# Kernel optimization log

Hardware: AMD Instinct MI355X
Metric: run time of the kernel (lower is better)

Reference implementation:

```python
import jax, jax.numpy as jnp
import numpy as np

N_NODES = 100000
N_EDGES = 3200000
D_IN = 128
D_HID = 32
D_OUT = 20
EPS = 1e-12  # matches torch F.normalize clamp


def setup_inputs() -> dict:
    key = jax.random.key(0)
    ks = jax.random.split(key, 10)
    x = jax.random.normal(ks[0], (N_NODES, D_IN), dtype=jnp.float32)
    edge_index = jax.random.randint(ks[1], (2, N_EDGES), 0, N_NODES, dtype=jnp.int32)
    def lin(k, fin, fout):
        return jax.random.normal(k, (fin, fout), dtype=jnp.float32) / np.float32(np.sqrt(fin))
    # SAGEConv: lin_l (applied to aggregated neighbors, has bias), lin_r (root, no bias)
    W1l = lin(ks[2], D_IN, D_HID); b1 = jnp.zeros((D_HID,), jnp.float32)
    W1r = lin(ks[3], D_IN, D_HID)
    W2l = lin(ks[4], D_HID, D_HID); b2 = jnp.zeros((D_HID,), jnp.float32)
    W2r = lin(ks[5], D_HID, D_HID)
    Wc = lin(ks[6], D_HID, D_OUT)
    bc = jax.random.normal(ks[7], (D_OUT,), dtype=jnp.float32) * 0.01
    return {"x": x, "edge_index": edge_index, "W1l": W1l, "b1": b1, "W1r": W1r,
            "W2l": W2l, "b2": b2, "W2r": W2r, "Wc": Wc, "bc": bc}


def _sage_conv(h, src, dst, Wl, bl, Wr):
    # mean aggregation of source features at destination nodes
    msgs = h[src]                                              # [E, d] gather
    agg = jax.ops.segment_sum(msgs, dst, num_segments=N_NODES)  # [N, d] scatter-add
    cnt = jax.ops.segment_sum(jnp.ones((src.shape[0],), h.dtype), dst, num_segments=N_NODES)
    mean = agg / jnp.maximum(cnt, 1.0)[:, None]
    out = mean @ Wl + bl + h @ Wr                              # combine neighbor + root
    norm = jnp.linalg.norm(out, axis=-1, keepdims=True)
    return out / jnp.maximum(norm, EPS)                        # L2 normalize


def reference(x, edge_index, W1l, b1, W1r, W2l, b2, W2r, Wc, bc):
    src, dst = edge_index[0], edge_index[1]
    h = jnp.tanh(_sage_conv(x, src, dst, W1l, b1, W1r))
    h = jnp.tanh(_sage_conv(h, src, dst, W2l, b2, W2r))
    out = jax.nn.log_softmax(h @ Wc + bc, axis=1)
    return (out, h)
```

## Files before the change

kernel.cpp:

```cpp
#include <hip/hip_runtime.h>
#include <hip/hip_fp16.h>
#include <cmath>

constexpr int NN   = 100000;
constexpr int NE   = 3200000;
constexpr int DIN  = 128;
constexpr int DH   = 32;
constexpr int DOUT = 20;

constexpr int NB    = 392;
constexpr int NBUSE = (NN + 255) / 256;
constexpr int NBLK  = 256;
constexpr int SLICE = NE / NBLK;

constexpr int NPB = 64;
constexpr int XSB = 136;
constexpr int HSS = 36;

typedef __attribute__((ext_vector_type(8))) short short8v;
typedef __attribute__((ext_vector_type(4))) float f32x4;

__device__ inline unsigned short f2bf(float f) {
    unsigned u = __builtin_bit_cast(unsigned, f);
    unsigned r = 0x7FFFu + ((u >> 16) & 1u);
    return (unsigned short)((u + r) >> 16);
}

__device__ inline unsigned f2fp8(float f) {
    unsigned u = __builtin_bit_cast(unsigned, f);
    unsigned s = (u >> 24) & 0x80u;
    unsigned au = u & 0x7fffffffu;
    if (au > 0x43E00000u) au = 0x43E00000u;
    unsigned u2 = au + 0x7FFFFu + ((au >> 20) & 1u);
    int em = (int)(u2 >> 20) - (120 << 3);
    em = em < 0 ? 0 : (em > 0x7E ? 0x7E : em);
    return s | (unsigned)em;
}
__device__ inline float dec8(unsigned b) {
    unsigned r = ((b & 0x80u) << 24) | (((b & 0x7fu) << 20) + 0x3C000000u);
    return __builtin_bit_cast(float, r);
}

__global__ __launch_bounds__(256, 4) void lin1_kernel(
    const float* __restrict__ x, const float* __restrict__ Wl,
    const float* __restrict__ Wr, unsigned char* __restrict__ xlf8,
    float* __restrict__ xr)
{
    __shared__ unsigned short xs[NPB * XSB];
    int t = threadIdx.x;
    int nodeBase = blockIdx.x * NPB;

    const float4* x4 = reinterpret_cast<const float4*>(x) + (size_t)nodeBase * (DIN / 4);
    for (int i = t; i < NPB * (DIN / 4); i += 256) {
        int n = i >> 5, c = i & 31;
        float4 v = make_float4(0.f, 0.f, 0.f, 0.f);
        if (nodeBase + n < NN) v = x4[i];
        unsigned lo = (unsigned)f2bf(v.x) | ((unsigned)f2bf(v.y) << 16);
        unsigned hi = (unsigned)f2bf(v.z) | ((unsigned)f2bf(v.w) << 16);
        *reinterpret_cast<uint2*>(&xs[n * XSB + c * 4]) = make_uint2(lo, hi);
    }
    __syncthreads();

    int wv   = t >> 6;
    int lane = t & 63;
    const float* W = (wv & 2) ? Wr : Wl;
    int jbase = (wv & 1) * 16;
    int ncol  = jbase + (lane & 15);
    int krow  = (lane >> 4) * 8;

    short8v bfrag[4];
#pragma unroll
    for (int ks = 0; ks < 4; ++ks) {
        const float* wp = W + (ks * 32 + krow) * DH + ncol;
        short8v f;
#pragma unroll
        for (int e = 0; e < 8; ++e) f[e] = (short)f2bf(wp[e * DH]);
        bfrag[ks] = f;
    }

    f32x4 acc[4];
#pragma unroll
    for (int m = 0; m < 4; ++m) acc[m] = f32x4{0.f, 0.f, 0.f, 0.f};

#pragma unroll
    for (int m = 0; m < 4; ++m) {
        int row = m * 16 + (lane & 15);
#pragma unroll
        for (int ks = 0; ks < 4; ++ks) {
            short8v a = *reinterpret_cast<const short8v*>(&xs[row * XSB + ks * 32 + krow]);
            acc[m] = __builtin_amdgcn_mfma_f32_16x16x32_bf16(a, bfrag[ks], acc[m], 0, 0, 0);
        }
    }

#pragma unroll
    for (int m = 0; m < 4; ++m) {
        int rbase = m * 16 + (lane >> 4) * 4;
#pragma unroll
        for (int r = 0; r < 4; ++r) {
            int node = nodeBase + rbase + r;
            if (node < NN) {
                float v = acc[m][r];
                if (wv & 2) xr[(size_t)node * DH + ncol] = v;
                else        xlf8[(size_t)node * DH + ncol] = (unsigned char)f2fp8(v);
            }
        }
    }
}

__global__ __launch_bounds__(1024) void countA_kernel(
    const int* __restrict__ ei, int* __restrict__ counts)
{
    __shared__ int h[NB];
    int blk = blockIdx.x, t = threadIdx.x;
    for (int i = t; i < NB; i += 1024) h[i] = 0;
    __syncthreads();
    int base = blk * SLICE;
    for (int i = base + t; i < base + SLICE; i += 1024) {
        int dst = ei[NE + i];
        atomicAdd(&h[dst >> 8], 1);
    }
    __syncthreads();
    for (int i = t; i < NB; i += 1024) counts[blk * NB + i] = h[i];
}

__global__ __launch_bounds__(256) void scanB1_kernel(
    const int* __restrict__ counts, int* __restrict__ offs, int* __restrict__ totals)
{
    __shared__ int sdata[256];
    int b = blockIdx.x, t = threadIdx.x;
    int v = counts[t * NB + b];
    int tp = (t & 7) * 32 + (t >> 3);
    sdata[tp] = v;
    __syncthreads();
    for (int off = 1; off < 256; off <<= 1) {
        int tmp = (t >= off) ? sdata[t - off] : 0;
        __syncthreads();
        sdata[t] += tmp;
        __syncthreads();
    }
    offs[b * 256 + t] = sdata[tp] - v;
    if (t == 255) totals[b] = sdata[255];
}

__global__ void scanB2_kernel(const int* __restrict__ totals, int* __restrict__ bases,
                              int* __restrict__ start)
{
    if (threadIdx.x == 0 && blockIdx.x == 0) {
        int acc = 0;
        for (int i = 0; i < NB; ++i) { bases[i] = acc; acc += totals[i]; }
        bases[NB] = acc;
        start[NN] = acc;
    }
}

__global__ __launch_bounds__(1024) void scatterC_kernel(
    const int* __restrict__ ei, const int* __restrict__ offs,
    const int* __restrict__ bases, unsigned* __restrict__ csrtmp)
{
    __shared__ int cnt[NB];
    __shared__ int wbase[NB];
    int blk = blockIdx.x, t = threadIdx.x;
    for (int i = t; i < NB; i += 1024) {
        cnt[i] = 0;
        wbase[i] = bases[i] + offs[i * 256 + blk];
    }
    __syncthreads();
    int base = blk * SLICE;
    for (int i = base + t; i < base + SLICE; i += 1024) {
        int dst = ei[NE + i];
        int src = ei[i];
        int b = dst >> 8;
        int r = atomicAdd(&cnt[b], 1);
        csrtmp[wbase[b] + r] = ((unsigned)(dst & 255) << 17) | (unsigned)src;
    }
}

__global__ __launch_bounds__(1024) void regroupD_kernel(
    const unsigned* __restrict__ csrtmp, const int* __restrict__ bases,
    int* __restrict__ csrsrc, int* __restrict__ start)
{
    __shared__ int h[256];
    __shared__ int sdata[256];
    int b = blockIdx.x, t = threadIdx.x;
    int lo = bases[b], hi = bases[b + 1];
    if (t < 256) h[t] = 0;
    __syncthreads();
    for (int i = lo + t; i < hi; i += 1024)
        atomicAdd(&h[csrtmp[i] >> 17], 1);
    __syncthreads();
    int v = 0;
    if (t < 256) { v = h[t]; sdata[t] = v; }
    __syncthreads();
    for (int off = 1; off < 256; off <<= 1) {
        int tmp = 0;
        if (t < 256 && t >= off) tmp = sdata[t - off];
        __syncthreads();
        if (t < 256) sdata[t] += tmp;
        __syncthreads();
    }
    if (t < 256) {
        int ex = sdata[t] - v;
        int node = b * 256 + t;
        if (node < NN) start[node] = lo + ex;
        h[t] = ex;
    }
    __syncthreads();
    for (int i = lo + t; i < hi; i += 1024) {
        unsigned u = csrtmp[i];
        int r = atomicAdd(&h[u >> 17], 1);
        csrsrc[lo + r] = (int)(u & 0x1FFFFu);
    }
}

__device__ inline float4 gather_core(const int* __restrict__ csrsrc,
                                     const unsigned* __restrict__ feat8,
                                     int s, int e, unsigned c)
{
    __half2 zero2 = __float2half2_rn(0.f);
    __half2 p0a = zero2, p0b = zero2, p1a = zero2, p1b = zero2;
    __half2 p2a = zero2, p2b = zero2, p3a = zero2, p3b = zero2;
    int i = s;
    for (; i + 8 <= e; i += 8) {
        unsigned off[8];
#pragma unroll
        for (int q = 0; q < 8; ++q) off[q] = (unsigned)csrsrc[i + q] * 8u + c;
        unsigned vv[8];
#pragma unroll
        for (int q = 0; q < 8; ++q) vv[q] = feat8[off[q]];
#pragma unroll
        for (int q = 0; q < 8; ++q) {
            unsigned w = vv[q];
            unsigned p01 = __builtin_amdgcn_perm(0u, w, 0x04010400u);
            unsigned p23 = __builtin_amdgcn_perm(0u, w, 0x04030402u);
            unsigned h01 = ((p01 & 0x00800080u) << 8) |
                           (((p01 << 7) & 0x3F803F80u) + 0x20002000u);
            unsigned h23 = ((p23 & 0x00800080u) << 8) |
                           (((p23 << 7) & 0x3F803F80u) + 0x20002000u);
            __half2 a01 = __builtin_bit_cast(__half2, h01);
            __half2 a23 = __builtin_bit_cast(__half2, h23);
            if ((q & 3) == 0) { p0a = __hadd2(p0a, a01); p0b = __hadd2(p0b, a23); }
            if ((q & 3) == 1) { p1a = __hadd2(p1a, a01); p1b = __hadd2(p1b, a23); }
            if ((q & 3) == 2) { p2a = __hadd2(p2a, a01); p2b = __hadd2(p2b, a23); }
            if ((q & 3) == 3) { p3a = __hadd2(p3a, a01); p3b = __hadd2(p3b, a23); }
        }
    }
    float4 tl = make_float4(0.f, 0.f, 0.f, 0.f);
    for (; i < e; ++i) {
        unsigned w = feat8[(unsigned)csrsrc[i] * 8u + c];
        tl.x += dec8(w & 0xFFu);         tl.y += dec8((w >> 8) & 0xFFu);
        tl.z += dec8((w >> 16) & 0xFFu); tl.w += dec8(w >> 24);
    }
    float2 f0a = __half22float2(p0a), f1a = __half22float2(p1a);
    float2 f2a = __half22float2(p2a), f3a = __half22float2(p3a);
    float2 f0b = __half22float2(p0b), f1b = __half22float2(p1b);
    float2 f2b = __half22float2(p2b), f3b = __half22float2(p3b);
    float4 r;
    r.x = tl.x + f0a.x + f1a.x + f2a.x + f3a.x;
    r.y = tl.y + f0a.y + f1a.y + f2a.y + f3a.y;
    r.z = tl.z + f0b.x + f1b.x + f2b.x + f3b.x;
    r.w = tl.w + f0b.y + f1b.y + f2b.y + f3b.y;
    return r;
}

__global__ __launch_bounds__(256) void fused1_kernel(
    const int* __restrict__ start, const int* __restrict__ csrsrc,
    const unsigned* __restrict__ feat8, const float* __restrict__ xr,
    const float* __restrict__ b1, const float* __restrict__ W2l,
    const float* __restrict__ W2r, unsigned* __restrict__ hlf8u,
    float* __restrict__ hr)
{
    __shared__ float hs[32][HSS];
    int tid = blockIdx.x * 256 + threadIdx.x;
    int g = tid >> 3;
    unsigned c = threadIdx.x & 7;
    int nl = threadIdx.x >> 3;

    int s = start[g];
    int e = start[g + 1];
    float4 r = gather_core(csrsrc, feat8, s, e, c);

    float inv = 1.0f / fmaxf((float)(e - s), 1.0f);
    const float4 root = *reinterpret_cast<const float4*>(xr + (size_t)g * DH + c * 4);
    const float4 bb   = *reinterpret_cast<const float4*>(b1 + c * 4);
    float4 o;
    o.x = fmaf(r.x, inv, bb.x + root.x);
    o.y = fmaf(r.y, inv, bb.y + root.y);
    o.z = fmaf(r.z, inv, bb.z + root.z);
    o.w = fmaf(r.w, inv, bb.w + root.w);

    float ss = o.x*o.x + o.y*o.y + o.z*o.z + o.w*o.w;
    ss += __shfl_xor(ss, 1);
    ss += __shfl_xor(ss, 2);
    ss += __shfl_xor(ss, 4);
    float rn = 1.0f / fmaxf(sqrtf(ss), 1e-12f);
    float4 h;
    h.x = tanhf(o.x * rn); h.y = tanhf(o.y * rn);
    h.z = tanhf(o.z * rn); h.w = tanhf(o.w * rn);
    *reinterpret_cast<float4*>(&hs[nl][c * 4]) = h;
    __syncthreads();

    float al[4] = {0.f, 0.f, 0.f, 0.f};
    float ar[4] = {0.f, 0.f, 0.f, 0.f};
#pragma unroll
    for (int k4 = 0; k4 < 8; ++k4) {
        float4 hv = *reinterpret_cast<const float4*>(&hs[nl][k4 * 4]);
        float hk[4] = {hv.x, hv.y, hv.z, hv.w};
#pragma unroll
        for (int kk = 0; kk < 4; ++kk) {
            const float4* wl4 = reinterpret_cast<const float4*>(W2l + (k4*4+kk) * DH + c * 4);
            const float4* wr4 = reinterpret_cast<const float4*>(W2r + (k4*4+kk) * DH + c * 4);
            float4 wl = wl4[0], wr = wr4[0];
            al[0] = fmaf(hk[kk], wl.x, al[0]);
            al[1] = fmaf(hk[kk], wl.y, al[1]);
            al[2] = fmaf(hk[kk], wl.z, al[2]);
            al[3] = fmaf(hk[kk], wl.w, al[3]);
            ar[0] = fmaf(hk[kk], wr.x, ar[0]);
            ar[1] = fmaf(hk[kk], wr.y, ar[1]);
            ar[2] = fmaf(hk[kk], wr.z, ar[2]);
            ar[3] = fmaf(hk[kk], wr.w, ar[3]);
        }
    }
    hlf8u[(size_t)g * 8 + c] = f2fp8(al[0]) | (f2fp8(al[1]) << 8) |
                               (f2fp8(al[2]) << 16) | (f2fp8(al[3]) << 24);
    *reinterpret_cast<float4*>(hr + (size_t)g * DH + c * 4) =
        make_float4(ar[0], ar[1], ar[2], ar[3]);
}

__global__ __launch_bounds__(256) void fused2_kernel(
    const int* __restrict__ start, const int* __restrict__ csrsrc,
    const unsigned* __restrict__ feat8, const float* __restrict__ hr,
    const float* __restrict__ b2, const float* __restrict__ Wc,
    const float* __restrict__ bc, float* __restrict__ h2out,
    float* __restrict__ outp)
{
    __shared__ float hs[32][HSS];
    int tid = blockIdx.x * 256 + threadIdx.x;
    int g = tid >> 3;
    unsigned c = threadIdx.x & 7;
    int nl = threadIdx.x >> 3;

    int s = start[g];
    int e = start[g + 1];
    float4 r = gather_core(csrsrc, feat8, s, e, c);

    float inv = 1.0f / fmaxf((float)(e - s), 1.0f);
    const float4 root = *reinterpret_cast<const float4*>(hr + (size_t)g * DH + c * 4);
    const float4 bb   = *reinterpret_cast<const float4*>(b2 + c * 4);
    float4 o;
    o.x = fmaf(r.x, inv, bb.x + root.x);
    o.y = fmaf(r.y, inv, bb.y + root.y);
    o.z = fmaf(r.z, inv, bb.z + root.z);
    o.w = fmaf(r.w, inv, bb.w + root.w);

    float ss = o.x*o.x + o.y*o.y + o.z*o.z + o.w*o.w;
    ss += __shfl_xor(ss, 1);
    ss += __shfl_xor(ss, 2);
    ss += __shfl_xor(ss, 4);
    float rn = 1.0f / fmaxf(sqrtf(ss), 1e-12f);
    float4 h;
    h.x = tanhf(o.x * rn); h.y = tanhf(o.y * rn);
    h.z = tanhf(o.z * rn); h.w = tanhf(o.w * rn);
    *reinterpret_cast<float4*>(&hs[nl][c * 4]) = h;
    *reinterpret_cast<float4*>(h2out + (size_t)g * DH + c * 4) = h;
    __syncthreads();

    if (c < 4) {
        float z[5];
#pragma unroll
        for (int q = 0; q < 5; ++q) z[q] = bc[c * 5 + q];
#pragma unroll
        for (int k4 = 0; k4 < 8; ++k4) {
            float4 hv = *reinterpret_cast<const float4*>(&hs[nl][k4 * 4]);
            float hk[4] = {hv.x, hv.y, hv.z, hv.w};
#pragma unroll
            for (int kk = 0; kk < 4; ++kk) {
                const float* wc = Wc + (k4*4+kk) * DOUT + c * 5;
#pragma unroll
                for (int q = 0; q < 5; ++q) z[q] = fmaf(hk[kk], wc[q], z[q]);
            }
        }
        float m = z[0];
#pragma unroll
        for (int q = 1; q < 5; ++q) m = fmaxf(m, z[q]);
        m = fmaxf(m, __shfl_xor(m, 1));
        m = fmaxf(m, __shfl_xor(m, 2));
        float sum = 0.f;
#pragma unroll
        for (int q = 0; q < 5; ++q) sum += expf(z[q] - m);
        sum += __shfl_xor(sum, 1);
        sum += __shfl_xor(sum, 2);
        float lse = m + logf(sum);
        float* orow = outp + (size_t)g * DOUT + c * 5;
#pragma unroll
        for (int q = 0; q < 5; ++q) orow[q] = z[q] - lse;
    }
}

extern "C" void kernel_launch(void* const* d_in, const int* in_sizes, int n_in,
                              void* d_out, int out_size, void* d_ws, size_t ws_size,
                              hipStream_t stream) {
    const float* x   = (const float*)d_in[0];
    const int*   ei  = (const int*)d_in[1];
    const float* W1l = (const float*)d_in[2];
    const float* b1  = (const float*)d_in[3];
    const float* W1r = (const float*)d_in[4];
    const float* W2l = (const float*)d_in[5];
    const float* b2  = (const float*)d_in[6];
    const float* W2r = (const float*)d_in[7];
    const float* Wc  = (const float*)d_in[8];
    const float* bc  = (const float*)d_in[9];

    float* outp = (float*)d_out;
    float* hout = outp + (size_t)NN * DOUT;

    unsigned char* xlf8 = (unsigned char*)d_ws;
    unsigned char* hlf8 = xlf8 + (size_t)NN * DH;
    float* xr      = (float*)(hlf8 + (size_t)NN * DH);
    unsigned* csrtmp = (unsigned*)(xr + (size_t)NN * DH);
    int* csrsrc    = (int*)(csrtmp + NE);
    int* start     = csrsrc + NE;
    int* counts    = start + NN + 1;
    int* offs      = counts + NBLK * NB;
    int* totals    = offs + NB * NBLK;
    int* bases     = totals + NB;

    const int lin1Blocks  = (NN + NPB - 1) / NPB;
    const int fusedBlocks = (NN * 8) / 256;

    lin1_kernel<<<lin1Blocks, 256, 0, stream>>>(x, W1l, W1r, xlf8, xr);

    countA_kernel<<<NBLK, 1024, 0, stream>>>(ei, counts);
    scanB1_kernel<<<NB, 256, 0, stream>>>(counts, offs, totals);
    scanB2_kernel<<<1, 64, 0, stream>>>(totals, bases, start);
    scatterC_kernel<<<NBLK, 1024, 0, stream>>>(ei, offs, bases, csrtmp);
    regroupD_kernel<<<NBUSE, 1024, 0, stream>>>(csrtmp, bases, csrsrc, start);

    fused1_kernel<<<fusedBlocks, 256, 0, stream>>>(start, csrsrc,
        (const unsigned*)xlf8, xr, b1, W2l, W2r, (unsigned*)hlf8, xr);

    fused2_kernel<<<fusedBlocks, 256, 0, stream>>>(start, csrsrc,
        (const unsigned*)hlf8, xr, b2, Wc, bc, hout, outp);
}
```

Measured before the change: 181.4 us.

## Sort nodes by degree to balance gather work across wavefronts

Adds a three-kernel counting sort (histogram, scan, scatter) that builds a permutation of nodes ordered by in-degree, capped at 255. Both fused aggregation kernels now take their node from this permutation, so each wavefront handles nodes with similar neighbour counts and idles less inside the gather loop. It also drops the block-level barriers before the shared-memory readback, relying on each node's 8 lanes sitting in the same wavefront. The cost is three extra launches, a small scan, and less contiguous access to per-node root, start and output arrays.

New measurement: 197.6 us. +9.0%, slower.

```diff
diff --git a/kernel.cpp b/kernel.cpp
--- a/kernel.cpp
+++ b/kernel.cpp
@@ -16,6 +16,7 @@
 constexpr int NPB = 64;
 constexpr int XSB = 136;
 constexpr int HSS = 36;
+constexpr int NSB = (NN + 1023) / 1024;
 
 typedef __attribute__((ext_vector_type(8))) short short8v;
 typedef __attribute__((ext_vector_type(4))) float f32x4;
@@ -209,6 +210,60 @@
         unsigned u = csrtmp[i];
         int r = atomicAdd(&h[u >> 17], 1);
         csrsrc[lo + r] = (int)(u & 0x1FFFFu);
+    }
+}
+
+__global__ __launch_bounds__(1024) void sortA_kernel(
+    const int* __restrict__ start, int* __restrict__ scounts)
+{
+    __shared__ int h[256];
+    int blk = blockIdx.x, t = threadIdx.x;
+    if (t < 256) h[t] = 0;
+    __syncthreads();
+    int node = blk * 1024 + t;
+    if (node < NN) {
+        int d = start[node + 1] - start[node];
+        int bin = d > 255 ? 255 : d;
+        atomicAdd(&h[bin], 1);
+    }
+    __syncthreads();
+    if (t < 256) scounts[blk * 256 + t] = h[t];
+}
+
+__global__ __launch_bounds__(256) void sortB_kernel(
+    const int* __restrict__ scounts, int* __restrict__ soffs)
+{
+    __shared__ int sdata[256];
+    int b = threadIdx.x;
+    int s = 0;
+    for (int k = 0; k < NSB; ++k) { soffs[b * NSB + k] = s; s += scounts[k * 256 + b]; }
+    sdata[b] = s;
+    __syncthreads();
+    for (int off = 1; off < 256; off <<= 1) {
+        int tmp = (b >= off) ? sdata[b - off] : 0;
+        __syncthreads();
+        sdata[b] += tmp;
+        __syncthreads();
+    }
+    int base = sdata[b] - s;
+    for (int k = 0; k < NSB; ++k) soffs[b * NSB + k] += base;
+}
+
+__global__ __launch_bounds__(1024) void sortC_kernel(
+    const int* __restrict__ start, const int* __restrict__ soffs,
+    int* __restrict__ perm)
+{
+    __shared__ int cnt[256];
+    __shared__ int wb[256];
+    int blk = blockIdx.x, t = threadIdx.x;
+    if (t < 256) { cnt[t] = 0; wb[t] = soffs[t * NSB + blk]; }
+    __syncthreads();
+    int node = blk * 1024 + t;
+    if (node < NN) {
+        int d = start[node + 1] - start[node];
+        int bin = d > 255 ? 255 : d;
+        int r = atomicAdd(&cnt[bin], 1);
+        perm[wb[bin] + r] = node;
     }
 }
 
@@ -263,15 +318,15 @@
 }
 
 __global__ __launch_bounds__(256) void fused1_kernel(
-    const int* __restrict__ start, const int* __restrict__ csrsrc,
-    const unsigned* __restrict__ feat8, const float* __restrict__ xr,
-    const float* __restrict__ b1, const float* __restrict__ W2l,
-    const float* __restrict__ W2r, unsigned* __restrict__ hlf8u,
-    float* __restrict__ hr)
+    const int* __restrict__ perm, const int* __restrict__ start,
+    const int* __restrict__ csrsrc, const unsigned* __restrict__ feat8,
+    const float* __restrict__ xr, const float* __restrict__ b1,
+    const float* __restrict__ W2l, const float* __restrict__ W2r,
+    unsigned* __restrict__ hlf8u, float* __restrict__ hr)
 {
     __shared__ float hs[32][HSS];
     int tid = blockIdx.x * 256 + threadIdx.x;
-    int g = tid >> 3;
+    int g = perm[tid >> 3];
     unsigned c = threadIdx.x & 7;
     int nl = threadIdx.x >> 3;
 
@@ -297,7 +352,6 @@
     h.x = tanhf(o.x * rn); h.y = tanhf(o.y * rn);
     h.z = tanhf(o.z * rn); h.w = tanhf(o.w * rn);
     *reinterpret_cast<float4*>(&hs[nl][c * 4]) = h;
-    __syncthreads();
 
     float al[4] = {0.f, 0.f, 0.f, 0.f};
     float ar[4] = {0.f, 0.f, 0.f, 0.f};
@@ -327,15 +381,15 @@
 }
 
 __global__ __launch_bounds__(256) void fused2_kernel(
-    const int* __restrict__ start, const int* __restrict__ csrsrc,
-    const unsigned* __restrict__ feat8, const float* __restrict__ hr,
-    const float* __restrict__ b2, const float* __restrict__ Wc,
-    const float* __restrict__ bc, float* __restrict__ h2out,
-    float* __restrict__ outp)
+    const int* __restrict__ perm, const int* __restrict__ start,
+    const int* __restrict__ csrsrc, const unsigned* __restrict__ feat8,
+    const float* __restrict__ hr, const float* __restrict__ b2,
+    const float* __restrict__ Wc, const float* __restrict__ bc,
+    float* __restrict__ h2out, float* __restrict__ outp)
 {
     __shared__ float hs[32][HSS];
     int tid = blockIdx.x * 256 + threadIdx.x;
-    int g = tid >> 3;
+    int g = perm[tid >> 3];
     unsigned c = threadIdx.x & 7;
     int nl = threadIdx.x >> 3;
 
@@ -362,7 +416,6 @@
     h.z = tanhf(o.z * rn); h.w = tanhf(o.w * rn);
     *reinterpret_cast<float4*>(&hs[nl][c * 4]) = h;
     *reinterpret_cast<float4*>(h2out + (size_t)g * DH + c * 4) = h;
-    __syncthreads();
 
     if (c < 4) {
         float z[5];
@@ -419,10 +472,13 @@
     unsigned* csrtmp = (unsigned*)(xr + (size_t)NN * DH);
     int* csrsrc    = (int*)(csrtmp + NE);
     int* start     = csrsrc + NE;
-    int* counts    = start + NN + 1;
+    int* perm      = start + NN + 1;
+    int* counts    = perm + NN;
     int* offs      = counts + NBLK * NB;
     int* totals    = offs + NB * NBLK;
     int* bases     = totals + NB;
+    int* scounts   = bases + NB + 1;
+    int* soffs     = scounts + NSB * 256;
 
     const int lin1Blocks  = (NN + NPB - 1) / NPB;
     const int fusedBlocks = (NN * 8) / 256;
@@ -435,9 +491,13 @@
     scatterC_kernel<<<NBLK, 1024, 0, stream>>>(ei, offs, bases, csrtmp);
     regroupD_kernel<<<NBUSE, 1024, 0, stream>>>(csrtmp, bases, csrsrc, start);
 
-    fused1_kernel<<<fusedBlocks, 256, 0, stream>>>(start, csrsrc,
+    sortA_kernel<<<NSB, 1024, 0, stream>>>(start, scounts);
+    sortB_kernel<<<1, 256, 0, stream>>>(scounts, soffs);
+    sortC_kernel<<<NSB, 1024, 0, stream>>>(start, soffs, perm);
+
+    fused1_kernel<<<fusedBlocks, 256, 0, stream>>>(perm, start, csrsrc,
         (const unsigned*)xlf8, xr, b1, W2l, W2r, (unsigned*)hlf8, xr);
 
-    fused2_kernel<<<fusedBlocks, 256, 0, stream>>>(start, csrsrc,
+    fused2_kernel<<<fusedBlocks, 256, 0, stream>>>(perm, start, csrsrc,
         (const unsigned*)hlf8, xr, b2, Wc, bc, hout, outp);
 }
```

## Sort nodes by degree within blocks to balance gather loops and trim decode

Applied to the files above, without the earlier changes.

Adds a small kernel that bitonic-sorts each group of 256 nodes by in-degree and writes a permutation. Both fused aggregation kernels take it, so the 8 nodes sharing a wavefront get similar neighbour-loop trip counts and less lane divergence. The fp8-to-half decode is shortened by letting an add carry the sign bit, and the block-wide barrier before the shared-memory matmul is dropped, relying on the 8 cooperating lanes being in the same wavefront. This costs an extra kernel launch and an extra indirection, and it scatters root loads and output stores slightly within each 256-node block.

Result: no change. 181.6 us (+0.1%).

```diff
diff --git a/kernel.cpp b/kernel.cpp
--- a/kernel.cpp
+++ b/kernel.cpp
@@ -212,6 +212,37 @@
     }
 }
 
+__global__ __launch_bounds__(256) void sortLocal_kernel(
+    const int* __restrict__ start, int* __restrict__ perm)
+{
+    __shared__ unsigned key[256];
+    int t = threadIdx.x;
+    int base = blockIdx.x * 256;
+    int g = base + t;
+    unsigned k;
+    if (g < NN) {
+        unsigned d = (unsigned)(start[g + 1] - start[g]);
+        k = (d << 9) | (unsigned)t;
+    } else {
+        k = 0xFFFFFE00u | (unsigned)t;
+    }
+    key[t] = k;
+    __syncthreads();
+    for (int sz = 2; sz <= 256; sz <<= 1) {
+        for (int str = sz >> 1; str > 0; str >>= 1) {
+            int p = t ^ str;
+            if (p > t) {
+                bool up = ((t & sz) == 0);
+                unsigned a = key[t], b = key[p];
+                if ((a > b) == up) { key[t] = b; key[p] = a; }
+            }
+            __syncthreads();
+        }
+    }
+    int node = base + (int)(key[t] & 0x1FFu);
+    if (g < NN && node < NN) perm[g] = node;
+}
+
 __device__ inline float4 gather_core(const int* __restrict__ csrsrc,
                                      const unsigned* __restrict__ feat8,
                                      int s, int e, unsigned c)
@@ -232,10 +263,8 @@
             unsigned w = vv[q];
             unsigned p01 = __builtin_amdgcn_perm(0u, w, 0x04010400u);
             unsigned p23 = __builtin_amdgcn_perm(0u, w, 0x04030402u);
-            unsigned h01 = ((p01 & 0x00800080u) << 8) |
-                           (((p01 << 7) & 0x3F803F80u) + 0x20002000u);
-            unsigned h23 = ((p23 & 0x00800080u) << 8) |
-                           (((p23 << 7) & 0x3F803F80u) + 0x20002000u);
+            unsigned h01 = (p01 << 7) + ((p01 & 0x00800080u) << 7) + 0x20002000u;
+            unsigned h23 = (p23 << 7) + ((p23 & 0x00800080u) << 7) + 0x20002000u;
             __half2 a01 = __builtin_bit_cast(__half2, h01);
             __half2 a23 = __builtin_bit_cast(__half2, h23);
             if ((q & 3) == 0) { p0a = __hadd2(p0a, a01); p0b = __hadd2(p0b, a23); }
@@ -263,15 +292,15 @@
 }
 
 __global__ __launch_bounds__(256) void fused1_kernel(
-    const int* __restrict__ start, const int* __restrict__ csrsrc,
-    const unsigned* __restrict__ feat8, const float* __restrict__ xr,
-    const float* __restrict__ b1, const float* __restrict__ W2l,
-    const float* __restrict__ W2r, unsigned* __restrict__ hlf8u,
-    float* __restrict__ hr)
+    const int* __restrict__ perm, const int* __restrict__ start,
+    const int* __restrict__ csrsrc, const unsigned* __restrict__ feat8,
+    const float* __restrict__ xr, const float* __restrict__ b1,
+    const float* __restrict__ W2l, const float* __restrict__ W2r,
+    unsigned* __restrict__ hlf8u, float* __restrict__ hr)
 {
     __shared__ float hs[32][HSS];
     int tid = blockIdx.x * 256 + threadIdx.x;
-    int g = tid >> 3;
+    int g = perm[tid >> 3];
     unsigned c = threadIdx.x & 7;
     int nl = threadIdx.x >> 3;
 
@@ -297,7 +326,6 @@
     h.x = tanhf(o.x * rn); h.y = tanhf(o.y * rn);
     h.z = tanhf(o.z * rn); h.w = tanhf(o.w * rn);
     *reinterpret_cast<float4*>(&hs[nl][c * 4]) = h;
-    __syncthreads();
 
     float al[4] = {0.f, 0.f, 0.f, 0.f};
     float ar[4] = {0.f, 0.f, 0.f, 0.f};
@@ -327,15 +355,15 @@
 }
 
 __global__ __launch_bounds__(256) void fused2_kernel(
-    const int* __restrict__ start, const int* __restrict__ csrsrc,
-    const unsigned* __restrict__ feat8, const float* __restrict__ hr,
-    const float* __restrict__ b2, const float* __restrict__ Wc,
-    const float* __restrict__ bc, float* __restrict__ h2out,
-    float* __restrict__ outp)
+    const int* __restrict__ perm, const int* __restrict__ start,
+    const int* __restrict__ csrsrc, const unsigned* __restrict__ feat8,
+    const float* __restrict__ hr, const float* __restrict__ b2,
+    const float* __restrict__ Wc, const float* __restrict__ bc,
+    float* __restrict__ h2out, float* __restrict__ outp)
 {
     __shared__ float hs[32][HSS];
     int tid = blockIdx.x * 256 + threadIdx.x;
-    int g = tid >> 3;
+    int g = perm[tid >> 3];
     unsigned c = threadIdx.x & 7;
     int nl = threadIdx.x >> 3;
 
@@ -362,7 +390,6 @@
     h.z = tanhf(o.z * rn); h.w = tanhf(o.w * rn);
     *reinterpret_cast<float4*>(&hs[nl][c * 4]) = h;
     *reinterpret_cast<float4*>(h2out + (size_t)g * DH + c * 4) = h;
-    __syncthreads();
 
     if (c < 4) {
         float z[5];
@@ -419,7 +446,8 @@
     unsigned* csrtmp = (unsigned*)(xr + (size_t)NN * DH);
     int* csrsrc    = (int*)(csrtmp + NE);
     int* start     = csrsrc + NE;
-    int* counts    = start + NN + 1;
+    int* perm      = start + NN + 1;
+    int* counts    = perm + NN;
     int* offs      = counts + NBLK * NB;
     int* totals    = offs + NB * NBLK;
     int* bases     = totals + NB;
@@ -435,9 +463,11 @@
     scatterC_kernel<<<NBLK, 1024, 0, stream>>>(ei, offs, bases, csrtmp);
     regroupD_kernel<<<NBUSE, 1024, 0, stream>>>(csrtmp, bases, csrsrc, start);
 
-    fused1_kernel<<<fusedBlocks, 256, 0, stream>>>(start, csrsrc,
+    sortLocal_kernel<<<NBUSE, 256, 0, stream>>>(start, perm);
+
+    fused1_kernel<<<fusedBlocks, 256, 0, stream>>>(perm, start, csrsrc,
         (const unsigned*)xlf8, xr, b1, W2l, W2r, (unsigned*)hlf8, xr);
 
-    fused2_kernel<<<fusedBlocks, 256, 0, stream>>>(start, csrsrc,
+    fused2_kernel<<<fusedBlocks, 256, 0, stream>>>(perm, start, csrsrc,
         (const unsigned*)hlf8, xr, b2, Wc, bc, hout, outp);
 }
```
